# Kernel optimization log

Measured on AMD Instinct MI355X. Metric: run time of the kernel, lower is better.

## Reference

```python
import jax, jax.numpy as jnp
import numpy as np

EPS = 1e-5  # torch LayerNorm default


def setup_inputs() -> dict:
    key = jax.random.key(0)
    ks = jax.random.split(key, 6)
    B, C, H, W, D = 8, 128, 64, 64, 32
    x = jax.random.normal(ks[0], (B, C, H, W), dtype=jnp.float32)
    gamma = jnp.ones((C,), dtype=jnp.float32)
    beta = jnp.zeros((C,), dtype=jnp.float32)
    Wq = jax.random.normal(ks[1], (D, C), dtype=jnp.float32) * 0.02
    Wk = jax.random.normal(ks[2], (D, C), dtype=jnp.float32) * 0.02
    Wv = jax.random.normal(ks[3], (C, C), dtype=jnp.float32) * 0.02
    Wo = jax.random.normal(ks[4], (C, C), dtype=jnp.float32) * (1.0 / np.sqrt(C))
    bo = jnp.zeros((C,), dtype=jnp.float32)
    return {"x": x, "gamma": gamma, "beta": beta, "Wq": Wq, "Wk": Wk,
            "Wv": Wv, "Wo": Wo, "bo": bo}


def reference(x, gamma, beta, Wq, Wk, Wv, Wo, bo):
    B, C, H, W = x.shape
    # LayerNorm over channel dim (applied in NHWC in the original)
    xn = x.transpose(0, 2, 3, 1)                       # [B,H,W,C]
    mu = xn.mean(-1, keepdims=True)
    var = ((xn - mu) ** 2).mean(-1, keepdims=True)
    xn = (xn - mu) * jax.lax.rsqrt(var + EPS) * gamma + beta
    xn = xn.transpose(0, 3, 1, 2)                      # [B,C,H,W]
    # 1x1-conv projections == channel matmuls
    q = jnp.einsum('dc,bchw->bdhw', Wq, xn)
    k = jnp.einsum('dc,bchw->bdhw', Wk, xn)
    v = jnp.einsum('oc,bchw->bohw', Wv, xn)
    # full spatial attention: scores [B,H,W,H,W], softmax over key positions
    scores = jnp.einsum('bchw,bcxy->bhwxy', q, k)
    scores = scores.reshape(B, H, W, H * W)
    attn = jax.nn.softmax(scores, axis=-1).reshape(B, H, W, H, W)
    out = jnp.einsum('bhwxy,bcxy->bchw', attn, v)
    out = jnp.einsum('oc,bchw->bohw', Wo, out) + bo[None, :, None, None]
    return out + x
```

## Files before the change

### kernel.cpp

```cpp
#include <hip/hip_runtime.h>


#define NB 8
#define CCH 128
#define NTOK 4096
#define DQK 32
#define KT 64
#define KHALF 2048

typedef __attribute__((ext_vector_type(8))) short bf16x8;
typedef __attribute__((ext_vector_type(4))) float f32x4;
typedef unsigned short u16;
typedef unsigned int u32;

static __device__ __forceinline__ f32x4 mfma16(bf16x8 a, bf16x8 b, f32x4 c) {
  return __builtin_amdgcn_mfma_f32_16x16x32_bf16(a, b, c, 0, 0, 0);
}
static __device__ __forceinline__ u16 f2bf(float f) {
  union { float f; u32 u; } cv; cv.f = f;
  u32 u = cv.u;
  u += 0x7fffu + ((u >> 16) & 1u);
  return (u16)(u >> 16);
}
static __device__ __forceinline__ float bf2f(u16 v) {
  union { u32 u; float f; } cv; cv.u = ((u32)v) << 16;
  return cv.f;
}
static __device__ __forceinline__ u32 cvtpk(float lo, float hi) {
  u32 d;
  asm("v_cvt_pk_bf16_f32 %0, %1, %2" : "=v"(d) : "v"(lo), "v"(hi));
  return d;
}
static __device__ __forceinline__ void gload16(const void* g, void* l) {
  __builtin_amdgcn_global_load_lds(
      (const __attribute__((address_space(1))) void*)g,
      (__attribute__((address_space(3))) void*)l, 16, 0, 0);
}

__global__ __launch_bounds__(256) void wconv_kernel(
    const float* __restrict__ Wq, const float* __restrict__ Wk,
    const float* __restrict__ Wv, const float* __restrict__ Wo,
    u16* __restrict__ wcomb) {
  int idx = blockIdx.x * 256 + threadIdx.x;
  int r = idx >> 7;
  float v;
  if (r < 32)        v = Wq[idx];
  else if (r < 64)   v = Wk[idx - 4096];
  else if (r < 192)  v = Wv[idx - 8192];
  else               v = Wo[idx - 24576];
  wcomb[idx] = f2bf(v);
}

__global__ __launch_bounds__(256) void ln_kernel(
    const float* __restrict__ x, const float* __restrict__ gamma,
    const float* __restrict__ beta, u16* __restrict__ xn) {
  __shared__ float tile[128][64];
  __shared__ float red[2][4][64];
  __shared__ u16   xt[64][130];
  int t = threadIdx.x;
  int lane = t & 63, cq = t >> 6;
  int b = blockIdx.x >> 6;
  int posb = (blockIdx.x & 63) << 6;
  const float* xb = x + ((size_t)b * CCH) * NTOK + posb;
  for (int i = 0; i < 32; ++i) {
    int c = cq * 32 + i;
    tile[c][lane] = xb[(size_t)c * NTOK + lane];
  }
  __syncthreads();
  float s = 0.f, s2 = 0.f;
  for (int i = 0; i < 32; ++i) {
    float v = tile[cq * 32 + i][lane];
    s += v; s2 += v * v;
  }
  red[0][cq][lane] = s; red[1][cq][lane] = s2;
  __syncthreads();
  float mu  = (red[0][0][lane] + red[0][1][lane] + red[0][2][lane] + red[0][3][lane]) * (1.f / 128.f);
  float ex2 = (red[1][0][lane] + red[1][1][lane] + red[1][2][lane] + red[1][3][lane]) * (1.f / 128.f);
  float rstd = rsqrtf(ex2 - mu * mu + 1e-5f);
  for (int i = 0; i < 32; ++i) {
    int c = cq * 32 + i;
    float v = (tile[c][lane] - mu) * rstd * gamma[c] + beta[c];
    xt[lane][c] = f2bf(v);
  }
  __syncthreads();
  u32* dst = (u32*)(xn + ((size_t)(b * NTOK + posb)) * CCH);
  for (int i = 0; i < 16; ++i) {
    int idx = i * 256 + t;
    int row = idx >> 6, col2 = idx & 63;
    dst[idx] = *(const u32*)&xt[row][col2 * 2];
  }
}

__global__ __launch_bounds__(256) void qkv_kernel(
    const u16* __restrict__ xn, const u16* __restrict__ wcomb,
    u16* __restrict__ Qg, u16* __restrict__ Kg, u16* __restrict__ Vt) {
  int t = threadIdx.x;
  int w = t >> 6, lane = t & 63;
  int row16 = lane & 15, kgrp = lane >> 4;
  int tok0 = blockIdx.x * 64;
  int tokA = tok0 + w * 16 + row16;
  bf16x8 af[4];
  for (int ks = 0; ks < 4; ++ks)
    af[ks] = *(const bf16x8*)&xn[(size_t)tokA * CCH + ks * 32 + kgrp * 8];
  f32x4 zero = {0.f, 0.f, 0.f, 0.f};
  f32x4 acc[12];
  for (int nt = 0; nt < 12; ++nt) {
    acc[nt] = zero;
    for (int ks = 0; ks < 4; ++ks) {
      bf16x8 bf = *(const bf16x8*)&wcomb[(size_t)(nt * 16 + row16) * CCH + ks * 32 + kgrp * 8];
      acc[nt] = mfma16(af[ks], bf, acc[nt]);
    }
  }
  int b = tok0 >> 12;
  for (int nt = 0; nt < 12; ++nt) {
    int col = nt * 16 + row16;
    for (int r = 0; r < 4; ++r) {
      int token = tok0 + w * 16 + kgrp * 4 + r;
      if (col < 32) {
        Qg[(size_t)token * DQK + col] = f2bf(acc[nt][r] * 1.44269504f);
      } else if (col < 64) {
        Kg[(size_t)token * DQK + (col - 32)] = f2bf(acc[nt][r]);
      } else {
        int tl = token & (NTOK - 1);
        int kp = (tl & ~31) | ((tl & 12) << 1) | ((tl & 16) >> 2) | (tl & 3);
        Vt[((size_t)b * CCH + (col - 64)) * NTOK + kp] = f2bf(acc[nt][r]);
      }
    }
  }
}

__global__ __launch_bounds__(256) void attn_kernel(
    const u16* __restrict__ Qg, const u16* __restrict__ Kg,
    const u16* __restrict__ Vt, u16* __restrict__ Op0, u16* __restrict__ Op1,
    float* __restrict__ lp) {
  __shared__ u16 lds[2][10240];
  int t = threadIdx.x;
  int w = t >> 6, lane = t & 63;
  int row16 = lane & 15, kgrp = lane >> 4;

  int logical = ((blockIdx.x & 7) << 6) | (blockIdx.x >> 3);
  int qblk = logical & 31;
  int half = (logical >> 5) & 1;
  int b = logical >> 6;
  int q0 = qblk * 128;
  int kt0 = half * KHALF;

  const u16* Qb = Qg + ((size_t)(b * NTOK + q0 + w * 32)) * DQK;
  bf16x8 qf0 = *(const bf16x8*)&Qb[(size_t)row16 * DQK + kgrp * 8];
  bf16x8 qf1 = *(const bf16x8*)&Qb[(size_t)(16 + row16) * DQK + kgrp * 8];

  int pr = t >> 3, e8 = t & 7;
  int korig = e8 ^ (pr & 7);
  int kkey = pr * 2 + (korig >> 2);
  int kfs = korig & 3;
  const u16* ksrc = Kg + (size_t)(b * NTOK + kt0 + kkey) * DQK + kfs * 8;
  int cV = t >> 3;
  int sV = e8 ^ (cV & 7);
  const u16* vsrc = Vt + ((size_t)b * CCH + cV) * NTOK + kt0 + sV * 8;

  int kdst = w * 512;
  int vdst = w * 512;

  f32x4 zero = {0.f, 0.f, 0.f, 0.f};
  f32x4 o0[8], o1[8];
#pragma unroll
  for (int i = 0; i < 8; ++i) { o0[i] = zero; o1[i] = zero; }
  float l0 = 0.f, l1 = 0.f;

  auto stage = [&](int bi, int tile) {
    const u16* kp_ = ksrc + (size_t)tile * (KT * DQK);
    gload16(kp_, &lds[bi][kdst]);
    const u16* vp_ = vsrc + tile * KT;
    gload16(vp_,          &lds[bi][2048 + vdst]);
    gload16(vp_ + 131072, &lds[bi][2048 + 2048 + vdst]);
    gload16(vp_ + 262144, &lds[bi][2048 + 4096 + vdst]);
    gload16(vp_ + 393216, &lds[bi][2048 + 6144 + vdst]);
  };

  auto compute = [&](int bi) {
    const u16* kb = &lds[bi][0];
    const u16* vb = &lds[bi][2048];
    f32x4 sa0[4], sa1[4];
#pragma unroll
    for (int nt = 0; nt < 4; ++nt) {
      int slot = (nt * 8 + (row16 >> 1)) * 8 +
                 ((((row16 & 1) << 2) + kgrp) ^ (row16 >> 1));
      bf16x8 kf = *(const bf16x8*)&kb[slot * 8];
      sa0[nt] = mfma16(kf, qf0, zero);
      sa1[nt] = mfma16(kf, qf1, zero);
    }
#pragma unroll
    for (int nt = 0; nt < 4; ++nt)
      for (int r = 0; r < 4; ++r) {
        float p0 = __builtin_amdgcn_exp2f(sa0[nt][r]);
        float p1 = __builtin_amdgcn_exp2f(sa1[nt][r]);
        sa0[nt][r] = p0; sa1[nt][r] = p1;
        l0 += p0; l1 += p1;
      }
    union PU { u32 d[4]; bf16x8 v; };
    PU pf0[2], pf1[2];
#pragma unroll
    for (int ks = 0; ks < 2; ++ks) {
      pf0[ks].d[0] = cvtpk(sa0[2 * ks][0], sa0[2 * ks][1]);
      pf0[ks].d[1] = cvtpk(sa0[2 * ks][2], sa0[2 * ks][3]);
      pf0[ks].d[2] = cvtpk(sa0[2 * ks + 1][0], sa0[2 * ks + 1][1]);
      pf0[ks].d[3] = cvtpk(sa0[2 * ks + 1][2], sa0[2 * ks + 1][3]);
      pf1[ks].d[0] = cvtpk(sa1[2 * ks][0], sa1[2 * ks][1]);
      pf1[ks].d[1] = cvtpk(sa1[2 * ks][2], sa1[2 * ks][3]);
      pf1[ks].d[2] = cvtpk(sa1[2 * ks + 1][0], sa1[2 * ks + 1][1]);
      pf1[ks].d[3] = cvtpk(sa1[2 * ks + 1][2], sa1[2 * ks + 1][3]);
    }
#pragma unroll
    for (int ks = 0; ks < 2; ++ks)
#pragma unroll
      for (int ntc = 0; ntc < 8; ++ntc) {
        int vslot = (ntc * 16 + row16) * 8 + (((ks << 2) + kgrp) ^ (row16 & 7));
        bf16x8 vf = *(const bf16x8*)&vb[vslot * 8];
        o0[ntc] = mfma16(pf0[ks].v, vf, o0[ntc]);
        o1[ntc] = mfma16(pf1[ks].v, vf, o1[ntc]);
      }
  };

  stage(0, 0);
  asm volatile("s_waitcnt vmcnt(0)" ::: "memory");
  __builtin_amdgcn_s_barrier();
  int cur = 0;
  for (int tile = 0; tile < 31; ++tile) {
    stage(cur ^ 1, tile + 1);
    compute(cur);
    asm volatile("s_waitcnt vmcnt(0)" ::: "memory");
    __builtin_amdgcn_s_barrier();
    cur ^= 1;
  }
  compute(cur);

  for (int mk = 16; mk <= 32; mk <<= 1) {
    l0 += __shfl_xor(l0, mk);
    l1 += __shfl_xor(l1, mk);
  }
  u16* Opw = half ? Op1 : Op0;
  int tokb = b * NTOK + q0 + w * 32;
#pragma unroll
  for (int r = 0; r < 4; ++r) {
    int tk0 = tokb + kgrp * 4 + r;
    int tk1 = tokb + 16 + kgrp * 4 + r;
#pragma unroll
    for (int ntc = 0; ntc < 8; ++ntc) {
      Opw[(size_t)tk0 * CCH + ntc * 16 + row16] = f2bf(o0[ntc][r]);
      Opw[(size_t)tk1 * CCH + ntc * 16 + row16] = f2bf(o1[ntc][r]);
    }
  }
  if (kgrp == 0) {
    lp[half * 32768 + tokb + row16] = l0;
    lp[half * 32768 + tokb + 16 + row16] = l1;
  }
}

__global__ __launch_bounds__(256) void out_kernel(
    const u16* __restrict__ Op0, const u16* __restrict__ Op1,
    const float* __restrict__ lp, const u16* __restrict__ wcomb,
    const float* __restrict__ bo, const float* __restrict__ x,
    float* __restrict__ out) {
  int t = threadIdx.x;
  int w = t >> 6, lane = t & 63;
  int row16 = lane & 15, kgrp = lane >> 4;
  int tok0 = blockIdx.x * 64;
  int b = tok0 >> 12, tloc = tok0 & (NTOK - 1);
  int tokA = tok0 + w * 16 + row16;
  float inv = 1.f / (lp[tokA] + lp[32768 + tokA]);
  bf16x8 af[4];
  for (int ks = 0; ks < 4; ++ks) {
    bf16x8 a0 = *(const bf16x8*)&Op0[(size_t)tokA * CCH + ks * 32 + kgrp * 8];
    bf16x8 a1 = *(const bf16x8*)&Op1[(size_t)tokA * CCH + ks * 32 + kgrp * 8];
    bf16x8 av;
    for (int j = 0; j < 8; ++j) {
      float f = (bf2f((u16)a0[j]) + bf2f((u16)a1[j])) * inv;
      av[j] = (short)f2bf(f);
    }
    af[ks] = av;
  }
  f32x4 zero = {0.f, 0.f, 0.f, 0.f};
  f32x4 acc[8];
  for (int nt = 0; nt < 8; ++nt) {
    acc[nt] = zero;
    for (int ks = 0; ks < 4; ++ks) {
      bf16x8 bf = *(const bf16x8*)&wcomb[(size_t)(192 + nt * 16 + row16) * CCH + ks * 32 + kgrp * 8];
      acc[nt] = mfma16(af[ks], bf, acc[nt]);
    }
  }
  for (int nt = 0; nt < 8; ++nt) {
    int cout = nt * 16 + row16;
    float bias = bo[cout];
    size_t base = ((size_t)b * CCH + cout) * NTOK + tloc + w * 16 + kgrp * 4;
    float4 xr = *(const float4*)&x[base];
    float4 ov;
    ov.x = acc[nt][0] + bias + xr.x;
    ov.y = acc[nt][1] + bias + xr.y;
    ov.z = acc[nt][2] + bias + xr.z;
    ov.w = acc[nt][3] + bias + xr.w;
    *(float4*)&out[base] = ov;
  }
}

extern "C" void kernel_launch(void* const* d_in, const int* in_sizes, int n_in,
                              void* d_out, int out_size, void* d_ws, size_t ws_size,
                              hipStream_t stream) {
  const float* x     = (const float*)d_in[0];
  const float* gamma = (const float*)d_in[1];
  const float* beta  = (const float*)d_in[2];
  const float* Wq    = (const float*)d_in[3];
  const float* Wk    = (const float*)d_in[4];
  const float* Wv    = (const float*)d_in[5];
  const float* Wo    = (const float*)d_in[6];
  const float* bo    = (const float*)d_in[7];
  float* out = (float*)d_out;

  unsigned char* ws = (unsigned char*)d_ws;
  u16* xn    = (u16*)(ws);
  u16* Qg    = (u16*)(ws + 8388608);
  u16* Kg    = (u16*)(ws + 10485760);
  u16* Vt    = (u16*)(ws + 12582912);
  u16* Op1   = (u16*)(ws + 20971520);
  float* lp  = (float*)(ws + 29360128);
  u16* wcomb = (u16*)(ws + 29622272);
  u16* Op0   = xn;

  wconv_kernel<<<160, 256, 0, stream>>>(Wq, Wk, Wv, Wo, wcomb);
  ln_kernel<<<512, 256, 0, stream>>>(x, gamma, beta, xn);
  qkv_kernel<<<512, 256, 0, stream>>>(xn, wcomb, Qg, Kg, Vt);
  attn_kernel<<<512, 256, 0, stream>>>(Qg, Kg, Vt, Op0, Op1, lp);
  out_kernel<<<512, 256, 0, stream>>>(Op0, Op1, lp, wcomb, bo, x, out);
}
```

Baseline: 101.3 us.

## Fuse LayerNorm into QKV projection and halve attention query tile

Merges the LayerNorm and QKV projection kernels so the normalized tile feeds the MFMA projection straight from shared memory, removing the xn global write and re-read and one launch. The attention kernel now gives each wave 16 queries instead of 32, with 64-query blocks and twice as many blocks (1024). It also adds a min-blocks-per-SM launch bound of 4. The smaller query tile is meant to cut registers and raise occupancy and parallelism. The cost is that each K/V tile loaded into LDS is reused by half as many queries, doubling total K/V traffic.

```diff
diff --git a/kernel.cpp b/kernel.cpp
--- a/kernel.cpp
+++ b/kernel.cpp
@@ -51,9 +51,10 @@
   wcomb[idx] = f2bf(v);
 }
 
-__global__ __launch_bounds__(256) void ln_kernel(
+__global__ __launch_bounds__(256) void lnqkv_kernel(
     const float* __restrict__ x, const float* __restrict__ gamma,
-    const float* __restrict__ beta, u16* __restrict__ xn) {
+    const float* __restrict__ beta, const u16* __restrict__ wcomb,
+    u16* __restrict__ Qg, u16* __restrict__ Kg, u16* __restrict__ Vt) {
   __shared__ float tile[128][64];
   __shared__ float red[2][4][64];
   __shared__ u16   xt[64][130];
@@ -83,25 +84,10 @@
     xt[lane][c] = f2bf(v);
   }
   __syncthreads();
-  u32* dst = (u32*)(xn + ((size_t)(b * NTOK + posb)) * CCH);
-  for (int i = 0; i < 16; ++i) {
-    int idx = i * 256 + t;
-    int row = idx >> 6, col2 = idx & 63;
-    dst[idx] = *(const u32*)&xt[row][col2 * 2];
-  }
-}
-
-__global__ __launch_bounds__(256) void qkv_kernel(
-    const u16* __restrict__ xn, const u16* __restrict__ wcomb,
-    u16* __restrict__ Qg, u16* __restrict__ Kg, u16* __restrict__ Vt) {
-  int t = threadIdx.x;
-  int w = t >> 6, lane = t & 63;
-  int row16 = lane & 15, kgrp = lane >> 4;
-  int tok0 = blockIdx.x * 64;
-  int tokA = tok0 + w * 16 + row16;
+  int w = t >> 6, row16 = lane & 15, kgrp = lane >> 4;
   bf16x8 af[4];
   for (int ks = 0; ks < 4; ++ks)
-    af[ks] = *(const bf16x8*)&xn[(size_t)tokA * CCH + ks * 32 + kgrp * 8];
+    af[ks] = *(const bf16x8*)&xt[w * 16 + row16][ks * 32 + kgrp * 8];
   f32x4 zero = {0.f, 0.f, 0.f, 0.f};
   f32x4 acc[12];
   for (int nt = 0; nt < 12; ++nt) {
@@ -111,7 +97,7 @@
       acc[nt] = mfma16(af[ks], bf, acc[nt]);
     }
   }
-  int b = tok0 >> 12;
+  int tok0 = b * NTOK + posb;
   for (int nt = 0; nt < 12; ++nt) {
     int col = nt * 16 + row16;
     for (int r = 0; r < 4; ++r) {
@@ -129,7 +115,7 @@
   }
 }
 
-__global__ __launch_bounds__(256) void attn_kernel(
+__global__ __launch_bounds__(256, 4) void attn_kernel(
     const u16* __restrict__ Qg, const u16* __restrict__ Kg,
     const u16* __restrict__ Vt, u16* __restrict__ Op0, u16* __restrict__ Op1,
     float* __restrict__ lp) {
@@ -138,16 +124,14 @@
   int w = t >> 6, lane = t & 63;
   int row16 = lane & 15, kgrp = lane >> 4;
 
-  int logical = ((blockIdx.x & 7) << 6) | (blockIdx.x >> 3);
-  int qblk = logical & 31;
-  int half = (logical >> 5) & 1;
-  int b = logical >> 6;
-  int q0 = qblk * 128;
+  int logical = ((blockIdx.x & 7) << 7) | (blockIdx.x >> 3);
+  int qblk = logical & 63;
+  int half = (logical >> 6) & 1;
+  int b = logical >> 7;
+  int q0 = qblk * 64;
   int kt0 = half * KHALF;
 
-  const u16* Qb = Qg + ((size_t)(b * NTOK + q0 + w * 32)) * DQK;
-  bf16x8 qf0 = *(const bf16x8*)&Qb[(size_t)row16 * DQK + kgrp * 8];
-  bf16x8 qf1 = *(const bf16x8*)&Qb[(size_t)(16 + row16) * DQK + kgrp * 8];
+  bf16x8 qf = *(const bf16x8*)&Qg[((size_t)(b * NTOK + q0 + w * 16 + row16)) * DQK + kgrp * 8];
 
   int pr = t >> 3, e8 = t & 7;
   int korig = e8 ^ (pr & 7);
@@ -162,10 +146,10 @@
   int vdst = w * 512;
 
   f32x4 zero = {0.f, 0.f, 0.f, 0.f};
-  f32x4 o0[8], o1[8];
-#pragma unroll
-  for (int i = 0; i < 8; ++i) { o0[i] = zero; o1[i] = zero; }
-  float l0 = 0.f, l1 = 0.f;
+  f32x4 o[8];
+#pragma unroll
+  for (int i = 0; i < 8; ++i) o[i] = zero;
+  float l0 = 0.f;
 
   auto stage = [&](int bi, int tile) {
     const u16* kp_ = ksrc + (size_t)tile * (KT * DQK);
@@ -180,35 +164,29 @@
   auto compute = [&](int bi) {
     const u16* kb = &lds[bi][0];
     const u16* vb = &lds[bi][2048];
-    f32x4 sa0[4], sa1[4];
+    f32x4 sa[4];
 #pragma unroll
     for (int nt = 0; nt < 4; ++nt) {
       int slot = (nt * 8 + (row16 >> 1)) * 8 +
                  ((((row16 & 1) << 2) + kgrp) ^ (row16 >> 1));
       bf16x8 kf = *(const bf16x8*)&kb[slot * 8];
-      sa0[nt] = mfma16(kf, qf0, zero);
-      sa1[nt] = mfma16(kf, qf1, zero);
+      sa[nt] = mfma16(kf, qf, zero);
     }
 #pragma unroll
     for (int nt = 0; nt < 4; ++nt)
       for (int r = 0; r < 4; ++r) {
-        float p0 = __builtin_amdgcn_exp2f(sa0[nt][r]);
-        float p1 = __builtin_amdgcn_exp2f(sa1[nt][r]);
-        sa0[nt][r] = p0; sa1[nt][r] = p1;
-        l0 += p0; l1 += p1;
+        float p0 = __builtin_amdgcn_exp2f(sa[nt][r]);
+        sa[nt][r] = p0;
+        l0 += p0;
       }
     union PU { u32 d[4]; bf16x8 v; };
-    PU pf0[2], pf1[2];
+    PU pf[2];
 #pragma unroll
     for (int ks = 0; ks < 2; ++ks) {
-      pf0[ks].d[0] = cvtpk(sa0[2 * ks][0], sa0[2 * ks][1]);
-      pf0[ks].d[1] = cvtpk(sa0[2 * ks][2], sa0[2 * ks][3]);
-      pf0[ks].d[2] = cvtpk(sa0[2 * ks + 1][0], sa0[2 * ks + 1][1]);
-      pf0[ks].d[3] = cvtpk(sa0[2 * ks + 1][2], sa0[2 * ks + 1][3]);
-      pf1[ks].d[0] = cvtpk(sa1[2 * ks][0], sa1[2 * ks][1]);
-      pf1[ks].d[1] = cvtpk(sa1[2 * ks][2], sa1[2 * ks][3]);
-      pf1[ks].d[2] = cvtpk(sa1[2 * ks + 1][0], sa1[2 * ks + 1][1]);
-      pf1[ks].d[3] = cvtpk(sa1[2 * ks + 1][2], sa1[2 * ks + 1][3]);
+      pf[ks].d[0] = cvtpk(sa[2 * ks][0], sa[2 * ks][1]);
+      pf[ks].d[1] = cvtpk(sa[2 * ks][2], sa[2 * ks][3]);
+      pf[ks].d[2] = cvtpk(sa[2 * ks + 1][0], sa[2 * ks + 1][1]);
+      pf[ks].d[3] = cvtpk(sa[2 * ks + 1][2], sa[2 * ks + 1][3]);
     }
 #pragma unroll
     for (int ks = 0; ks < 2; ++ks)
@@ -216,8 +194,7 @@
       for (int ntc = 0; ntc < 8; ++ntc) {
         int vslot = (ntc * 16 + row16) * 8 + (((ks << 2) + kgrp) ^ (row16 & 7));
         bf16x8 vf = *(const bf16x8*)&vb[vslot * 8];
-        o0[ntc] = mfma16(pf0[ks].v, vf, o0[ntc]);
-        o1[ntc] = mfma16(pf1[ks].v, vf, o1[ntc]);
+        o[ntc] = mfma16(pf[ks].v, vf, o[ntc]);
       }
   };
 
@@ -234,26 +211,19 @@
   }
   compute(cur);
 
-  for (int mk = 16; mk <= 32; mk <<= 1) {
+  for (int mk = 16; mk <= 32; mk <<= 1)
     l0 += __shfl_xor(l0, mk);
-    l1 += __shfl_xor(l1, mk);
-  }
   u16* Opw = half ? Op1 : Op0;
-  int tokb = b * NTOK + q0 + w * 32;
+  int tokb = b * NTOK + q0 + w * 16;
 #pragma unroll
   for (int r = 0; r < 4; ++r) {
-    int tk0 = tokb + kgrp * 4 + r;
-    int tk1 = tokb + 16 + kgrp * 4 + r;
-#pragma unroll
-    for (int ntc = 0; ntc < 8; ++ntc) {
-      Opw[(size_t)tk0 * CCH + ntc * 16 + row16] = f2bf(o0[ntc][r]);
-      Opw[(size_t)tk1 * CCH + ntc * 16 + row16] = f2bf(o1[ntc][r]);
-    }
-  }
-  if (kgrp == 0) {
+    int tk = tokb + kgrp * 4 + r;
+#pragma unroll
+    for (int ntc = 0; ntc < 8; ++ntc)
+      Opw[(size_t)tk * CCH + ntc * 16 + row16] = f2bf(o[ntc][r]);
+  }
+  if (kgrp == 0)
     lp[half * 32768 + tokb + row16] = l0;
-    lp[half * 32768 + tokb + 16 + row16] = l1;
-  }
 }
 
 __global__ __launch_bounds__(256) void out_kernel(
@@ -316,18 +286,16 @@
   float* out = (float*)d_out;
 
   unsigned char* ws = (unsigned char*)d_ws;
-  u16* xn    = (u16*)(ws);
+  u16* Op0   = (u16*)(ws);
   u16* Qg    = (u16*)(ws + 8388608);
   u16* Kg    = (u16*)(ws + 10485760);
   u16* Vt    = (u16*)(ws + 12582912);
   u16* Op1   = (u16*)(ws + 20971520);
   float* lp  = (float*)(ws + 29360128);
   u16* wcomb = (u16*)(ws + 29622272);
-  u16* Op0   = xn;
 
   wconv_kernel<<<160, 256, 0, stream>>>(Wq, Wk, Wv, Wo, wcomb);
-  ln_kernel<<<512, 256, 0, stream>>>(x, gamma, beta, xn);
-  qkv_kernel<<<512, 256, 0, stream>>>(xn, wcomb, Qg, Kg, Vt);
-  attn_kernel<<<512, 256, 0, stream>>>(Qg, Kg, Vt, Op0, Op1, lp);
+  lnqkv_kernel<<<512, 256, 0, stream>>>(x, gamma, beta, wcomb, Qg, Kg, Vt);
+  attn_kernel<<<1024, 256, 0, stream>>>(Qg, Kg, Vt, Op0, Op1, lp);
   out_kernel<<<512, 256, 0, stream>>>(Op0, Op1, lp, wcomb, bo, x, out);
 }
```

Result: faster. 93.80 us (-7.4%).

## Fuse LayerNorm with QKV projection and split attention keys four ways

Applied to the files above, without the earlier changes.

Merges the LayerNorm and QKV projection kernels so the normalized activations stay in LDS and are never written to or read back from global memory. Attention now splits the key range into four segments when the workspace is large enough, giving 1024 blocks instead of 512 for better CU occupancy, at the cost of more partial outputs for the final kernel to sum. Row sums of the softmax numerator are now computed with an extra MFMA against a ones vector instead of scalar adds and shuffles, and launch bounds request 4 blocks per CU.

```diff
diff --git a/kernel.cpp b/kernel.cpp
--- a/kernel.cpp
+++ b/kernel.cpp
@@ -6,7 +6,6 @@
 #define NTOK 4096
 #define DQK 32
 #define KT 64
-#define KHALF 2048
 
 typedef __attribute__((ext_vector_type(8))) short bf16x8;
 typedef __attribute__((ext_vector_type(4))) float f32x4;
@@ -51,9 +50,10 @@
   wcomb[idx] = f2bf(v);
 }
 
-__global__ __launch_bounds__(256) void ln_kernel(
+__global__ __launch_bounds__(256) void lnqkv_kernel(
     const float* __restrict__ x, const float* __restrict__ gamma,
-    const float* __restrict__ beta, u16* __restrict__ xn) {
+    const float* __restrict__ beta, const u16* __restrict__ wcomb,
+    u16* __restrict__ Qg, u16* __restrict__ Kg, u16* __restrict__ Vt) {
   __shared__ float tile[128][64];
   __shared__ float red[2][4][64];
   __shared__ u16   xt[64][130];
@@ -83,25 +83,10 @@
     xt[lane][c] = f2bf(v);
   }
   __syncthreads();
-  u32* dst = (u32*)(xn + ((size_t)(b * NTOK + posb)) * CCH);
-  for (int i = 0; i < 16; ++i) {
-    int idx = i * 256 + t;
-    int row = idx >> 6, col2 = idx & 63;
-    dst[idx] = *(const u32*)&xt[row][col2 * 2];
-  }
-}
-
-__global__ __launch_bounds__(256) void qkv_kernel(
-    const u16* __restrict__ xn, const u16* __restrict__ wcomb,
-    u16* __restrict__ Qg, u16* __restrict__ Kg, u16* __restrict__ Vt) {
-  int t = threadIdx.x;
-  int w = t >> 6, lane = t & 63;
-  int row16 = lane & 15, kgrp = lane >> 4;
-  int tok0 = blockIdx.x * 64;
-  int tokA = tok0 + w * 16 + row16;
+  int w = t >> 6, row16 = lane & 15, kgrp = lane >> 4;
   bf16x8 af[4];
   for (int ks = 0; ks < 4; ++ks)
-    af[ks] = *(const bf16x8*)&xn[(size_t)tokA * CCH + ks * 32 + kgrp * 8];
+    af[ks] = *(const bf16x8*)&xt[w * 16 + row16][ks * 32 + kgrp * 8];
   f32x4 zero = {0.f, 0.f, 0.f, 0.f};
   f32x4 acc[12];
   for (int nt = 0; nt < 12; ++nt) {
@@ -111,7 +96,7 @@
       acc[nt] = mfma16(af[ks], bf, acc[nt]);
     }
   }
-  int b = tok0 >> 12;
+  int tok0 = b * NTOK + posb;
   for (int nt = 0; nt < 12; ++nt) {
     int col = nt * 16 + row16;
     for (int r = 0; r < 4; ++r) {
@@ -129,25 +114,37 @@
   }
 }
 
-__global__ __launch_bounds__(256) void attn_kernel(
+template <int NS>
+__global__ __launch_bounds__(256, 4) void attn_kernel(
     const u16* __restrict__ Qg, const u16* __restrict__ Kg,
-    const u16* __restrict__ Vt, u16* __restrict__ Op0, u16* __restrict__ Op1,
+    const u16* __restrict__ Vt, u16* __restrict__ Op,
     float* __restrict__ lp) {
   __shared__ u16 lds[2][10240];
+  constexpr int KSEG = NTOK / NS;
+  constexpr int NTILE = KSEG / KT;
+  constexpr int BSH = (NS == 4) ? 7 : 6;
   int t = threadIdx.x;
   int w = t >> 6, lane = t & 63;
   int row16 = lane & 15, kgrp = lane >> 4;
 
-  int logical = ((blockIdx.x & 7) << 6) | (blockIdx.x >> 3);
+  int cpx = (256 * NS) >> 3;
+  int logical = (blockIdx.x & 7) * cpx + (blockIdx.x >> 3);
   int qblk = logical & 31;
-  int half = (logical >> 5) & 1;
-  int b = logical >> 6;
+  int part = (logical >> 5) & (NS - 1);
+  int b = logical >> BSH;
   int q0 = qblk * 128;
-  int kt0 = half * KHALF;
+  int kt0 = part * KSEG;
 
   const u16* Qb = Qg + ((size_t)(b * NTOK + q0 + w * 32)) * DQK;
   bf16x8 qf0 = *(const bf16x8*)&Qb[(size_t)row16 * DQK + kgrp * 8];
   bf16x8 qf1 = *(const bf16x8*)&Qb[(size_t)(16 + row16) * DQK + kgrp * 8];
+
+  bf16x8 ones_b;
+  {
+    short one = (short)0x3F80;
+    short val = (row16 == 0) ? one : (short)0;
+    for (int j = 0; j < 8; ++j) ones_b[j] = val;
+  }
 
   int pr = t >> 3, e8 = t & 7;
   int korig = e8 ^ (pr & 7);
@@ -162,10 +159,10 @@
   int vdst = w * 512;
 
   f32x4 zero = {0.f, 0.f, 0.f, 0.f};
-  f32x4 o0[8], o1[8];
+  f32x4 o0[8], o1[8], ol0, ol1;
 #pragma unroll
   for (int i = 0; i < 8; ++i) { o0[i] = zero; o1[i] = zero; }
-  float l0 = 0.f, l1 = 0.f;
+  ol0 = zero; ol1 = zero;
 
   auto stage = [&](int bi, int tile) {
     const u16* kp_ = ksrc + (size_t)tile * (KT * DQK);
@@ -192,10 +189,8 @@
 #pragma unroll
     for (int nt = 0; nt < 4; ++nt)
       for (int r = 0; r < 4; ++r) {
-        float p0 = __builtin_amdgcn_exp2f(sa0[nt][r]);
-        float p1 = __builtin_amdgcn_exp2f(sa1[nt][r]);
-        sa0[nt][r] = p0; sa1[nt][r] = p1;
-        l0 += p0; l1 += p1;
+        sa0[nt][r] = __builtin_amdgcn_exp2f(sa0[nt][r]);
+        sa1[nt][r] = __builtin_amdgcn_exp2f(sa1[nt][r]);
       }
     union PU { u32 d[4]; bf16x8 v; };
     PU pf0[2], pf1[2];
@@ -210,6 +205,10 @@
       pf1[ks].d[2] = cvtpk(sa1[2 * ks + 1][0], sa1[2 * ks + 1][1]);
       pf1[ks].d[3] = cvtpk(sa1[2 * ks + 1][2], sa1[2 * ks + 1][3]);
     }
+    ol0 = mfma16(pf0[0].v, ones_b, ol0);
+    ol0 = mfma16(pf0[1].v, ones_b, ol0);
+    ol1 = mfma16(pf1[0].v, ones_b, ol1);
+    ol1 = mfma16(pf1[1].v, ones_b, ol1);
 #pragma unroll
     for (int ks = 0; ks < 2; ++ks)
 #pragma unroll
@@ -225,7 +224,7 @@
   asm volatile("s_waitcnt vmcnt(0)" ::: "memory");
   __builtin_amdgcn_s_barrier();
   int cur = 0;
-  for (int tile = 0; tile < 31; ++tile) {
+  for (int tile = 0; tile < NTILE - 1; ++tile) {
     stage(cur ^ 1, tile + 1);
     compute(cur);
     asm volatile("s_waitcnt vmcnt(0)" ::: "memory");
@@ -234,11 +233,7 @@
   }
   compute(cur);
 
-  for (int mk = 16; mk <= 32; mk <<= 1) {
-    l0 += __shfl_xor(l0, mk);
-    l1 += __shfl_xor(l1, mk);
-  }
-  u16* Opw = half ? Op1 : Op0;
+  u16* Opw = Op + (size_t)part * (32768 * CCH);
   int tokb = b * NTOK + q0 + w * 32;
 #pragma unroll
   for (int r = 0; r < 4; ++r) {
@@ -250,33 +245,38 @@
       Opw[(size_t)tk1 * CCH + ntc * 16 + row16] = f2bf(o1[ntc][r]);
     }
   }
-  if (kgrp == 0) {
-    lp[half * 32768 + tokb + row16] = l0;
-    lp[half * 32768 + tokb + 16 + row16] = l1;
+  if (row16 == 0) {
+#pragma unroll
+    for (int r = 0; r < 4; ++r) {
+      lp[part * 32768 + tokb + kgrp * 4 + r] = ol0[r];
+      lp[part * 32768 + tokb + 16 + kgrp * 4 + r] = ol1[r];
+    }
   }
 }
 
 __global__ __launch_bounds__(256) void out_kernel(
-    const u16* __restrict__ Op0, const u16* __restrict__ Op1,
-    const float* __restrict__ lp, const u16* __restrict__ wcomb,
-    const float* __restrict__ bo, const float* __restrict__ x,
-    float* __restrict__ out) {
+    const u16* __restrict__ Op, const float* __restrict__ lp, int ns,
+    const u16* __restrict__ wcomb, const float* __restrict__ bo,
+    const float* __restrict__ x, float* __restrict__ out) {
   int t = threadIdx.x;
   int w = t >> 6, lane = t & 63;
   int row16 = lane & 15, kgrp = lane >> 4;
   int tok0 = blockIdx.x * 64;
   int b = tok0 >> 12, tloc = tok0 & (NTOK - 1);
   int tokA = tok0 + w * 16 + row16;
-  float inv = 1.f / (lp[tokA] + lp[32768 + tokA]);
+  float lsum = 0.f;
+  for (int j = 0; j < ns; ++j) lsum += lp[j * 32768 + tokA];
+  float inv = 1.f / lsum;
   bf16x8 af[4];
   for (int ks = 0; ks < 4; ++ks) {
-    bf16x8 a0 = *(const bf16x8*)&Op0[(size_t)tokA * CCH + ks * 32 + kgrp * 8];
-    bf16x8 a1 = *(const bf16x8*)&Op1[(size_t)tokA * CCH + ks * 32 + kgrp * 8];
+    float sum[8] = {0.f, 0.f, 0.f, 0.f, 0.f, 0.f, 0.f, 0.f};
+    for (int j = 0; j < ns; ++j) {
+      bf16x8 a = *(const bf16x8*)&Op[(size_t)j * (32768 * CCH) +
+                                     (size_t)tokA * CCH + ks * 32 + kgrp * 8];
+      for (int e = 0; e < 8; ++e) sum[e] += bf2f((u16)a[e]);
+    }
     bf16x8 av;
-    for (int j = 0; j < 8; ++j) {
-      float f = (bf2f((u16)a0[j]) + bf2f((u16)a1[j])) * inv;
-      av[j] = (short)f2bf(f);
-    }
+    for (int e = 0; e < 8; ++e) av[e] = (short)f2bf(sum[e] * inv);
     af[ks] = av;
   }
   f32x4 zero = {0.f, 0.f, 0.f, 0.f};
@@ -316,18 +316,20 @@
   float* out = (float*)d_out;
 
   unsigned char* ws = (unsigned char*)d_ws;
-  u16* xn    = (u16*)(ws);
-  u16* Qg    = (u16*)(ws + 8388608);
-  u16* Kg    = (u16*)(ws + 10485760);
-  u16* Vt    = (u16*)(ws + 12582912);
-  u16* Op1   = (u16*)(ws + 20971520);
-  float* lp  = (float*)(ws + 29360128);
-  u16* wcomb = (u16*)(ws + 29622272);
-  u16* Op0   = xn;
+  u16* Qg    = (u16*)(ws);
+  u16* Kg    = (u16*)(ws + 2097152);
+  u16* Vt    = (u16*)(ws + 4194304);
+  u16* wcomb = (u16*)(ws + 12582912);
+  float* lp  = (float*)(ws + 12664832);
+  u16* Op    = (u16*)(ws + 13189120);
+
+  int ns = (ws_size >= 46743552u) ? 4 : 2;
 
   wconv_kernel<<<160, 256, 0, stream>>>(Wq, Wk, Wv, Wo, wcomb);
-  ln_kernel<<<512, 256, 0, stream>>>(x, gamma, beta, xn);
-  qkv_kernel<<<512, 256, 0, stream>>>(xn, wcomb, Qg, Kg, Vt);
-  attn_kernel<<<512, 256, 0, stream>>>(Qg, Kg, Vt, Op0, Op1, lp);
-  out_kernel<<<512, 256, 0, stream>>>(Op0, Op1, lp, wcomb, bo, x, out);
-}
+  lnqkv_kernel<<<512, 256, 0, stream>>>(x, gamma, beta, wcomb, Qg, Kg, Vt);
+  if (ns == 4)
+    attn_kernel<4><<<1024, 256, 0, stream>>>(Qg, Kg, Vt, Op, lp);
+  else
+    attn_kernel<2><<<512, 256, 0, stream>>>(Qg, Kg, Vt, Op, lp);
+  out_kernel<<<512, 256, 0, stream>>>(Op, lp, ns, wcomb, bo, x, out);
+}
```

After: 93.34 us (median of 2 runs). 1.09x faster.
